# Optimization experiments

Hardware: AMD Instinct MI355X
Metric: run time of the kernel (lower is better)

The kernel has to match this reference:

```python
import jax, jax.numpy as jnp
import numpy as np

B, N, D, H, R, K = 64, 197, 768, 3072, 16, 1


def setup_inputs() -> dict:
    key = jax.random.key(0)
    ks = jax.random.split(key, 9)
    s1 = 1.0 / np.sqrt(D)
    s2 = 1.0 / np.sqrt(H)
    return {
        "x": jax.random.normal(ks[0], (B, N, D), dtype=jnp.float32),
        "W1": jax.random.normal(ks[1], (H, D), dtype=jnp.float32) * s1,
        "b1": jax.random.normal(ks[2], (H,), dtype=jnp.float32) * s1,
        "A1": jax.random.normal(ks[3], (K, R, D), dtype=jnp.float32) * s1,
        "B1": jax.random.normal(ks[4], (K, H, R), dtype=jnp.float32) * 0.01,
        "W2": jax.random.normal(ks[5], (D, H), dtype=jnp.float32) * s2,
        "b2": jax.random.normal(ks[6], (D,), dtype=jnp.float32) * s2,
        "A2": jax.random.normal(ks[7], (K, R, H), dtype=jnp.float32) * s2,
        "B2": jax.random.normal(ks[8], (K, D, R), dtype=jnp.float32) * 0.01,
    }


def _lora(x, A, Bm):
    # result of torch: (B @ (A @ x^T.unsqueeze(1))).sum(1).transpose(1,2)
    # A: [K, r, d_in], Bm: [K, d_out, r], x: [b, n, d_in] -> [b, n, d_out]
    t = jnp.einsum('krd,bnd->bknr', A, x)          # low-rank projection
    return jnp.einsum('kor,bknr->bno', Bm, t)      # expand + sum over K


def reference(x, W1, b1, A1, B1, W2, b2, A2, B2):
    # fc1 (Linear + LoRA correction)
    h = jnp.einsum('bnd,hd->bnh', x, W1) + b1 + _lora(x, A1, B1)
    # exact (erf-based) GELU, matching torch nn.GELU default
    h = jax.nn.gelu(h, approximate=False)
    # dropout p=0 and norm=Identity by default -> no-ops
    out = jnp.einsum('bnh,dh->bnd', h, W2) + b2 + _lora(h, A2, B2)
    return out
```

## Files before the change

### kernel.cpp

```cpp
#include <hip/hip_runtime.h>
#include <math.h>

#define M_ROWS 12608
#define D_DIM  768
#define H_DIM  3072

typedef __bf16 bf16_t;
typedef __bf16 bf16x8 __attribute__((ext_vector_type(8)));
typedef float  f32x4  __attribute__((ext_vector_type(4)));

__device__ __forceinline__ float gelu_fast(float v) {
  float v2 = v * v;
  float z = v * fmaf(0.044715f, v2, 1.0f);
  float e = __expf(-1.5957691216057308f * z);
  return v * __builtin_amdgcn_rcpf(1.0f + e);
}

__global__ void cast_f32_bf16_kernel(const float* __restrict__ in,
                                     bf16_t* __restrict__ out, long n) {
  long i = ((long)blockIdx.x * 256 + threadIdx.x) * 16;
  if (i + 15 < n) {
    float4 v[4];
#pragma unroll
    for (int q = 0; q < 4; ++q) v[q] = *(const float4*)(in + i + q * 4);
    bf16_t ov[16];
#pragma unroll
    for (int q = 0; q < 4; ++q) {
      ov[q * 4 + 0] = (bf16_t)v[q].x; ov[q * 4 + 1] = (bf16_t)v[q].y;
      ov[q * 4 + 2] = (bf16_t)v[q].z; ov[q * 4 + 3] = (bf16_t)v[q].w;
    }
    *(bf16x8*)(out + i) = *(bf16x8*)ov;
    *(bf16x8*)(out + i + 8) = *(bf16x8*)(ov + 8);
  } else {
    for (; i < n; ++i) out[i] = (bf16_t)in[i];
  }
}

__global__ void fold_lora_kernel(const float* __restrict__ W,
                                 const float* __restrict__ A,
                                 const float* __restrict__ Bm,
                                 bf16_t* __restrict__ Weff,
                                 int OUT, int IN) {
  const int nseg = IN >> 3;
  long idx = (long)blockIdx.x * 256 + threadIdx.x;
  if (idx >= (long)OUT * nseg) return;
  int o = (int)(idx / nseg);
  int s = (int)(idx - (long)o * nseg);
  const float* wp = W + (size_t)o * IN + s * 8;
  float4 w0 = *(const float4*)wp, w1 = *(const float4*)(wp + 4);
  float acc[8] = {w0.x, w0.y, w0.z, w0.w, w1.x, w1.y, w1.z, w1.w};
  float4 b4[4];
#pragma unroll
  for (int q = 0; q < 4; ++q) b4[q] = *(const float4*)(Bm + o * 16 + q * 4);
  const float* bb = (const float*)b4;
#pragma unroll
  for (int r = 0; r < 16; ++r) {
    float b = bb[r];
    const float* ap = A + (size_t)r * IN + s * 8;
    float4 a0 = *(const float4*)ap, a1 = *(const float4*)(ap + 4);
    acc[0] = fmaf(b, a0.x, acc[0]); acc[1] = fmaf(b, a0.y, acc[1]);
    acc[2] = fmaf(b, a0.z, acc[2]); acc[3] = fmaf(b, a0.w, acc[3]);
    acc[4] = fmaf(b, a1.x, acc[4]); acc[5] = fmaf(b, a1.y, acc[5]);
    acc[6] = fmaf(b, a1.z, acc[6]); acc[7] = fmaf(b, a1.w, acc[7]);
  }
  bf16_t ov[8];
#pragma unroll
  for (int i = 0; i < 8; ++i) ov[i] = (bf16_t)acc[i];
  *(bf16x8*)(Weff + (size_t)o * IN + s * 8) = *(bf16x8*)ov;
}

template <bool GELU, typename OutT, int SCHED>
__global__ __launch_bounds__(256, 2) void gemm_kernel(
    const bf16_t* __restrict__ Amat, const bf16_t* __restrict__ Bmat,
    const float* __restrict__ bias, OutT* __restrict__ Cmat,
    int Mrows, int Ncols, int Kd) {
  __shared__ char smem[65536];
  bf16_t* lds = (bf16_t*)smem;
  float* sT = (float*)smem;

  int rowb, colb;
  const int xcd = blockIdx.x & 7, t = blockIdx.x >> 3;
  if (SCHED == 1) {
    colb = t / 13;
    rowb = (t % 13) * 8 + xcd;
    if (rowb >= 99) return;
  } else {
    rowb = (t / 3) * 4 + (xcd & 3);
    if (rowb >= 99) return;
    colb = (xcd >> 2) * 3 + (t % 3);
  }
  const int row0 = rowb * 128, col0 = colb * 128;

  const int tid = threadIdx.x, lane = tid & 63, wave = tid >> 6;
  const int wm = wave & 1, wn = wave >> 1;

  const bf16_t* gA[4]; const bf16_t* gB[4];
  int offA[4], offB[4];
#pragma unroll
  for (int q = 0; q < 4; ++q) {
    int c = tid + q * 256;
    int r = c >> 3, kkg = c & 7;
    int ra = row0 + r; if (ra > Mrows - 1) ra = Mrows - 1;
    gA[q] = Amat + (size_t)ra * Kd + kkg * 8;
    offA[q] = r * 64 + (kkg ^ (r & 7)) * 8;
    gB[q] = Bmat + (size_t)(col0 + r) * Kd + kkg * 8;
    offB[q] = 8192 + r * 64 + (kkg ^ (r & 7)) * 8;
  }

  const int rl = lane & 15, kc = lane >> 4;
  int aoffs[4], boffs[4];
#pragma unroll
  for (int i = 0; i < 4; ++i) {
    int ra = wm * 64 + i * 16 + rl;
    int rb = wn * 64 + i * 16 + rl;
    aoffs[i] = ra * 64 + ((kc ^ (ra & 7)) * 8);
    boffs[i] = 8192 + rb * 64 + ((kc ^ (rb & 7)) * 8);
  }

  f32x4 acc[4][4] = {};
  f32x4 pA[4], pB[4];
  const int iters = Kd / 64;

#pragma unroll
  for (int q = 0; q < 4; ++q) {
    pA[q] = *(const f32x4*)gA[q]; pB[q] = *(const f32x4*)gB[q];
    gA[q] += 64; gB[q] += 64;
  }
#pragma unroll
  for (int q = 0; q < 4; ++q) {
    *(f32x4*)(lds + offA[q]) = pA[q];
    *(f32x4*)(lds + offB[q]) = pB[q];
  }

  for (int it = 0; it < iters; ++it) {
    const bool more = (it + 1 < iters);
    if (more) {
#pragma unroll
      for (int q = 0; q < 4; ++q) {
        pA[q] = *(const f32x4*)gA[q]; pB[q] = *(const f32x4*)gB[q];
        gA[q] += 64; gB[q] += 64;
      }
    }
    __syncthreads();
    const bf16_t* buf = lds + (it & 1) * 16384;
#pragma unroll
    for (int ks = 0; ks < 2; ++ks) {
      bf16x8 af[4], bfr[4];
#pragma unroll
      for (int i = 0; i < 4; ++i) af[i] = *(const bf16x8*)(buf + (aoffs[i] ^ (ks * 32)));
#pragma unroll
      for (int i = 0; i < 4; ++i) bfr[i] = *(const bf16x8*)(buf + (boffs[i] ^ (ks * 32)));
#pragma unroll
      for (int mi = 0; mi < 4; ++mi)
#pragma unroll
        for (int ni = 0; ni < 4; ++ni)
          acc[mi][ni] = __builtin_amdgcn_mfma_f32_16x16x32_bf16(
              af[mi], bfr[ni], acc[mi][ni], 0, 0, 0);
    }
    if (more) {
      bf16_t* nbuf = lds + ((it + 1) & 1) * 16384;
#pragma unroll
      for (int q = 0; q < 4; ++q) {
        *(f32x4*)(nbuf + offA[q]) = pA[q];
        *(f32x4*)(nbuf + offB[q]) = pB[q];
      }
    }
  }

  const int crow = (lane >> 4) * 4, ccol = lane & 15;
  if constexpr (GELU) {
    __syncthreads();
#pragma unroll
    for (int p = 0; p < 2; ++p) {
#pragma unroll
      for (int s = 0; s < 2; ++s) {
        int mi = 2 * p + s;
#pragma unroll
        for (int ni = 0; ni < 4; ++ni)
#pragma unroll
          for (int r = 0; r < 4; ++r)
            sT[(wm * 32 + s * 16 + crow + r) * 132 + wn * 64 + ni * 16 + ccol] =
                acc[mi][ni][r];
      }
      __syncthreads();
      const int erow = tid >> 2, eseg = tid & 3;
      const int grow = row0 + (erow >> 5) * 64 + (2 * p + ((erow >> 4) & 1)) * 16 + (erow & 15);
      if (grow < Mrows) {
        const float* src = sT + erow * 132 + eseg * 32;
        const float* bsrc = bias + col0 + eseg * 32;
        bf16_t ov[32];
#pragma unroll
        for (int i = 0; i < 32; ++i)
          ov[i] = (bf16_t)gelu_fast(src[i] + bsrc[i]);
        bf16_t* dst = (bf16_t*)Cmat + (size_t)grow * Ncols + col0 + eseg * 32;
#pragma unroll
        for (int k = 0; k < 4; ++k)
          *(bf16x8*)(dst + k * 8) = *(bf16x8*)(ov + k * 8);
      }
      __syncthreads();
    }
  } else {
#pragma unroll
    for (int ni = 0; ni < 4; ++ni) {
      const int gc = col0 + wn * 64 + ni * 16 + ccol;
      const float bv = bias[gc];
#pragma unroll
      for (int mi = 0; mi < 4; ++mi) {
        const int gr = row0 + wm * 64 + mi * 16 + crow;
#pragma unroll
        for (int r = 0; r < 4; ++r) {
          const int row = gr + r;
          if (row < Mrows)
            Cmat[(size_t)row * Ncols + gc] = acc[mi][ni][r] + bv;
        }
      }
    }
  }
}

extern "C" void kernel_launch(void* const* d_in, const int* in_sizes, int n_in,
                              void* d_out, int out_size, void* d_ws, size_t ws_size,
                              hipStream_t stream) {
  const float* x  = (const float*)d_in[0];
  const float* W1 = (const float*)d_in[1];
  const float* b1 = (const float*)d_in[2];
  const float* A1 = (const float*)d_in[3];
  const float* B1 = (const float*)d_in[4];
  const float* W2 = (const float*)d_in[5];
  const float* b2 = (const float*)d_in[6];
  const float* A2 = (const float*)d_in[7];
  const float* B2 = (const float*)d_in[8];
  float* out = (float*)d_out;

  char* ws = (char*)d_ws;
  bf16_t* xb    = (bf16_t*)ws;
  bf16_t* W1eff = (bf16_t*)(ws + 19366144);
  bf16_t* W2eff = (bf16_t*)(ws + 19366144 + 4718592);
  bf16_t* hbuf  = (bf16_t*)(ws + 19366144 + 2 * 4718592);

  const long nx = (long)M_ROWS * D_DIM;
  cast_f32_bf16_kernel<<<(int)(nx / 16 / 256 + 1), 256, 0, stream>>>(x, xb, nx);

  fold_lora_kernel<<<1152, 256, 0, stream>>>(W1, A1, B1, W1eff, H_DIM, D_DIM);
  fold_lora_kernel<<<1152, 256, 0, stream>>>(W2, A2, B2, W2eff, D_DIM, H_DIM);

  gemm_kernel<true, bf16_t, 1><<<2496, 256, 0, stream>>>(
      xb, W1eff, b1, hbuf, M_ROWS, H_DIM, D_DIM);
  gemm_kernel<false, float, 2><<<600, 256, 0, stream>>>(
      hbuf, W2eff, b2, out, M_ROWS, D_DIM, H_DIM);
}
```

Before: 319.9 us.

## Load A fragments directly from global, single-buffer B in LDS, fuse prep kernels

The GEMM now loads A-operand MFMA fragments straight from global memory into registers instead of staging them through LDS. Only B goes through LDS, now single-buffered with two barriers per iteration. That shrinks shared memory enough to raise launch bounds to 3 blocks per CU. The cast and two LoRA-fold kernels are merged into one prep launch to cut launch overhead. The risk is that uncoalesced per-lane global A loads and the extra barriers may stall the MFMA pipeline.

```diff
diff --git a/kernel.cpp b/kernel.cpp
--- a/kernel.cpp
+++ b/kernel.cpp
@@ -16,34 +16,29 @@
   return v * __builtin_amdgcn_rcpf(1.0f + e);
 }
 
-__global__ void cast_f32_bf16_kernel(const float* __restrict__ in,
-                                     bf16_t* __restrict__ out, long n) {
-  long i = ((long)blockIdx.x * 256 + threadIdx.x) * 16;
-  if (i + 15 < n) {
-    float4 v[4];
-#pragma unroll
-    for (int q = 0; q < 4; ++q) v[q] = *(const float4*)(in + i + q * 4);
-    bf16_t ov[16];
-#pragma unroll
-    for (int q = 0; q < 4; ++q) {
-      ov[q * 4 + 0] = (bf16_t)v[q].x; ov[q * 4 + 1] = (bf16_t)v[q].y;
-      ov[q * 4 + 2] = (bf16_t)v[q].z; ov[q * 4 + 3] = (bf16_t)v[q].w;
-    }
-    *(bf16x8*)(out + i) = *(bf16x8*)ov;
-    *(bf16x8*)(out + i + 8) = *(bf16x8*)(ov + 8);
-  } else {
-    for (; i < n; ++i) out[i] = (bf16_t)in[i];
-  }
-}
-
-__global__ void fold_lora_kernel(const float* __restrict__ W,
-                                 const float* __restrict__ A,
-                                 const float* __restrict__ Bm,
-                                 bf16_t* __restrict__ Weff,
-                                 int OUT, int IN) {
+__device__ __forceinline__ void cast16(const float* __restrict__ in,
+                                       bf16_t* __restrict__ out, int blk) {
+  long i = ((long)blk * 256 + threadIdx.x) * 16;
+  float4 v[4];
+#pragma unroll
+  for (int q = 0; q < 4; ++q) v[q] = *(const float4*)(in + i + q * 4);
+  bf16_t ov[16];
+#pragma unroll
+  for (int q = 0; q < 4; ++q) {
+    ov[q * 4 + 0] = (bf16_t)v[q].x; ov[q * 4 + 1] = (bf16_t)v[q].y;
+    ov[q * 4 + 2] = (bf16_t)v[q].z; ov[q * 4 + 3] = (bf16_t)v[q].w;
+  }
+  *(bf16x8*)(out + i) = *(bf16x8*)ov;
+  *(bf16x8*)(out + i + 8) = *(bf16x8*)(ov + 8);
+}
+
+__device__ __forceinline__ void fold8(const float* __restrict__ W,
+                                      const float* __restrict__ A,
+                                      const float* __restrict__ Bm,
+                                      bf16_t* __restrict__ Weff,
+                                      int IN, int blk) {
   const int nseg = IN >> 3;
-  long idx = (long)blockIdx.x * 256 + threadIdx.x;
-  if (idx >= (long)OUT * nseg) return;
+  long idx = (long)blk * 256 + threadIdx.x;
   int o = (int)(idx / nseg);
   int s = (int)(idx - (long)o * nseg);
   const float* wp = W + (size_t)o * IN + s * 8;
@@ -69,12 +64,23 @@
   *(bf16x8*)(Weff + (size_t)o * IN + s * 8) = *(bf16x8*)ov;
 }
 
-template <bool GELU, typename OutT, int SCHED>
-__global__ __launch_bounds__(256, 2) void gemm_kernel(
+__global__ void prep_kernel(const float* __restrict__ x, bf16_t* __restrict__ xb,
+                            const float* __restrict__ W1, const float* __restrict__ A1,
+                            const float* __restrict__ B1, bf16_t* __restrict__ W1eff,
+                            const float* __restrict__ W2, const float* __restrict__ A2,
+                            const float* __restrict__ B2, bf16_t* __restrict__ W2eff) {
+  int b = blockIdx.x;
+  if (b < 2364) cast16(x, xb, b);
+  else if (b < 3516) fold8(W1, A1, B1, W1eff, D_DIM, b - 2364);
+  else fold8(W2, A2, B2, W2eff, H_DIM, b - 3516);
+}
+
+template <bool GELU, typename OutT, int SCHED, int SMEM_BYTES>
+__global__ __launch_bounds__(256, 3) void gemm_kernel(
     const bf16_t* __restrict__ Amat, const bf16_t* __restrict__ Bmat,
     const float* __restrict__ bias, OutT* __restrict__ Cmat,
     int Mrows, int Ncols, int Kd) {
-  __shared__ char smem[65536];
+  __shared__ char smem[SMEM_BYTES];
   bf16_t* lds = (bf16_t*)smem;
   float* sT = (float*)smem;
 
@@ -93,77 +99,75 @@
 
   const int tid = threadIdx.x, lane = tid & 63, wave = tid >> 6;
   const int wm = wave & 1, wn = wave >> 1;
-
-  const bf16_t* gA[4]; const bf16_t* gB[4];
-  int offA[4], offB[4];
+  const int rl = lane & 15, kc = lane >> 4;
+
+  const bf16_t* aP[4];
+#pragma unroll
+  for (int mi = 0; mi < 4; ++mi) {
+    int r = row0 + wm * 64 + mi * 16 + rl;
+    if (r > Mrows - 1) r = Mrows - 1;
+    aP[mi] = Amat + (size_t)r * Kd + kc * 8;
+  }
+
+  const bf16_t* gB[4];
+  int offB[4];
 #pragma unroll
   for (int q = 0; q < 4; ++q) {
     int c = tid + q * 256;
     int r = c >> 3, kkg = c & 7;
-    int ra = row0 + r; if (ra > Mrows - 1) ra = Mrows - 1;
-    gA[q] = Amat + (size_t)ra * Kd + kkg * 8;
-    offA[q] = r * 64 + (kkg ^ (r & 7)) * 8;
     gB[q] = Bmat + (size_t)(col0 + r) * Kd + kkg * 8;
-    offB[q] = 8192 + r * 64 + (kkg ^ (r & 7)) * 8;
-  }
-
-  const int rl = lane & 15, kc = lane >> 4;
-  int aoffs[4], boffs[4];
+    offB[q] = r * 64 + (kkg ^ (r & 7)) * 8;
+  }
+
+  int boffs[4];
 #pragma unroll
   for (int i = 0; i < 4; ++i) {
-    int ra = wm * 64 + i * 16 + rl;
     int rb = wn * 64 + i * 16 + rl;
-    aoffs[i] = ra * 64 + ((kc ^ (ra & 7)) * 8);
-    boffs[i] = 8192 + rb * 64 + ((kc ^ (rb & 7)) * 8);
+    boffs[i] = rb * 64 + ((kc ^ (rb & 7)) * 8);
   }
 
   f32x4 acc[4][4] = {};
-  f32x4 pA[4], pB[4];
+  f32x4 pB[4];
   const int iters = Kd / 64;
 
 #pragma unroll
-  for (int q = 0; q < 4; ++q) {
-    pA[q] = *(const f32x4*)gA[q]; pB[q] = *(const f32x4*)gB[q];
-    gA[q] += 64; gB[q] += 64;
-  }
-#pragma unroll
-  for (int q = 0; q < 4; ++q) {
-    *(f32x4*)(lds + offA[q]) = pA[q];
-    *(f32x4*)(lds + offB[q]) = pB[q];
-  }
+  for (int q = 0; q < 4; ++q) { pB[q] = *(const f32x4*)gB[q]; gB[q] += 64; }
+#pragma unroll
+  for (int q = 0; q < 4; ++q) *(f32x4*)(lds + offB[q]) = pB[q];
+  __syncthreads();
 
   for (int it = 0; it < iters; ++it) {
     const bool more = (it + 1 < iters);
     if (more) {
 #pragma unroll
-      for (int q = 0; q < 4; ++q) {
-        pA[q] = *(const f32x4*)gA[q]; pB[q] = *(const f32x4*)gB[q];
-        gA[q] += 64; gB[q] += 64;
-      }
-    }
-    __syncthreads();
-    const bf16_t* buf = lds + (it & 1) * 16384;
+      for (int q = 0; q < 4; ++q) { pB[q] = *(const f32x4*)gB[q]; gB[q] += 64; }
+    }
+    bf16x8 af[4][2];
+#pragma unroll
+    for (int mi = 0; mi < 4; ++mi) {
+      af[mi][0] = *(const bf16x8*)(aP[mi]);
+      af[mi][1] = *(const bf16x8*)(aP[mi] + 32);
+      aP[mi] += 64;
+    }
 #pragma unroll
     for (int ks = 0; ks < 2; ++ks) {
-      bf16x8 af[4], bfr[4];
-#pragma unroll
-      for (int i = 0; i < 4; ++i) af[i] = *(const bf16x8*)(buf + (aoffs[i] ^ (ks * 32)));
-#pragma unroll
-      for (int i = 0; i < 4; ++i) bfr[i] = *(const bf16x8*)(buf + (boffs[i] ^ (ks * 32)));
+      bf16x8 bfr[4];
+#pragma unroll
+      for (int i = 0; i < 4; ++i)
+        bfr[i] = *(const bf16x8*)(lds + (boffs[i] ^ (ks * 32)));
 #pragma unroll
       for (int mi = 0; mi < 4; ++mi)
 #pragma unroll
         for (int ni = 0; ni < 4; ++ni)
           acc[mi][ni] = __builtin_amdgcn_mfma_f32_16x16x32_bf16(
-              af[mi], bfr[ni], acc[mi][ni], 0, 0, 0);
+              af[mi][ks], bfr[ni], acc[mi][ni], 0, 0, 0);
     }
     if (more) {
-      bf16_t* nbuf = lds + ((it + 1) & 1) * 16384;
-#pragma unroll
-      for (int q = 0; q < 4; ++q) {
-        *(f32x4*)(nbuf + offA[q]) = pA[q];
-        *(f32x4*)(nbuf + offB[q]) = pB[q];
-      }
+      __syncthreads();
+#pragma unroll
+      for (int q = 0; q < 4; ++q)
+        *(f32x4*)(lds + offB[q]) = pB[q];
+      __syncthreads();
     }
   }
 
@@ -238,14 +242,11 @@
   bf16_t* W2eff = (bf16_t*)(ws + 19366144 + 4718592);
   bf16_t* hbuf  = (bf16_t*)(ws + 19366144 + 2 * 4718592);
 
-  const long nx = (long)M_ROWS * D_DIM;
-  cast_f32_bf16_kernel<<<(int)(nx / 16 / 256 + 1), 256, 0, stream>>>(x, xb, nx);
-
-  fold_lora_kernel<<<1152, 256, 0, stream>>>(W1, A1, B1, W1eff, H_DIM, D_DIM);
-  fold_lora_kernel<<<1152, 256, 0, stream>>>(W2, A2, B2, W2eff, D_DIM, H_DIM);
-
-  gemm_kernel<true, bf16_t, 1><<<2496, 256, 0, stream>>>(
+  prep_kernel<<<4668, 256, 0, stream>>>(x, xb, W1, A1, B1, W1eff,
+                                        W2, A2, B2, W2eff);
+
+  gemm_kernel<true, bf16_t, 1, 33792><<<2496, 256, 0, stream>>>(
       xb, W1eff, b1, hbuf, M_ROWS, H_DIM, D_DIM);
-  gemm_kernel<false, float, 2><<<600, 256, 0, stream>>>(
+  gemm_kernel<false, float, 2, 16384><<<600, 256, 0, stream>>>(
       hbuf, W2eff, b2, out, M_ROWS, D_DIM, H_DIM);
 }
```

Result: slower. 459.4 us (+43.6%).

## Single-buffer GEMM LDS to raise occupancy and fuse prep kernels

Applied to the files above, without the earlier changes.

Merges the x cast and both LoRA fold kernels into one prep launch. The GEMM drops LDS double buffering, which cuts shared memory from 64KB to about 32KB per block, and raises the launch bounds to 3 blocks per CU. This trades the overlap of LDS writes with MFMA work for an extra barrier per K step, in return for higher occupancy and fewer launches.

```diff
diff --git a/kernel.cpp b/kernel.cpp
--- a/kernel.cpp
+++ b/kernel.cpp
@@ -16,34 +16,29 @@
   return v * __builtin_amdgcn_rcpf(1.0f + e);
 }
 
-__global__ void cast_f32_bf16_kernel(const float* __restrict__ in,
-                                     bf16_t* __restrict__ out, long n) {
-  long i = ((long)blockIdx.x * 256 + threadIdx.x) * 16;
-  if (i + 15 < n) {
-    float4 v[4];
-#pragma unroll
-    for (int q = 0; q < 4; ++q) v[q] = *(const float4*)(in + i + q * 4);
-    bf16_t ov[16];
-#pragma unroll
-    for (int q = 0; q < 4; ++q) {
-      ov[q * 4 + 0] = (bf16_t)v[q].x; ov[q * 4 + 1] = (bf16_t)v[q].y;
-      ov[q * 4 + 2] = (bf16_t)v[q].z; ov[q * 4 + 3] = (bf16_t)v[q].w;
-    }
-    *(bf16x8*)(out + i) = *(bf16x8*)ov;
-    *(bf16x8*)(out + i + 8) = *(bf16x8*)(ov + 8);
-  } else {
-    for (; i < n; ++i) out[i] = (bf16_t)in[i];
-  }
-}
-
-__global__ void fold_lora_kernel(const float* __restrict__ W,
-                                 const float* __restrict__ A,
-                                 const float* __restrict__ Bm,
-                                 bf16_t* __restrict__ Weff,
-                                 int OUT, int IN) {
+__device__ __forceinline__ void cast16(const float* __restrict__ in,
+                                       bf16_t* __restrict__ out, int blk) {
+  long i = ((long)blk * 256 + threadIdx.x) * 16;
+  float4 v[4];
+#pragma unroll
+  for (int q = 0; q < 4; ++q) v[q] = *(const float4*)(in + i + q * 4);
+  bf16_t ov[16];
+#pragma unroll
+  for (int q = 0; q < 4; ++q) {
+    ov[q * 4 + 0] = (bf16_t)v[q].x; ov[q * 4 + 1] = (bf16_t)v[q].y;
+    ov[q * 4 + 2] = (bf16_t)v[q].z; ov[q * 4 + 3] = (bf16_t)v[q].w;
+  }
+  *(bf16x8*)(out + i) = *(bf16x8*)ov;
+  *(bf16x8*)(out + i + 8) = *(bf16x8*)(ov + 8);
+}
+
+__device__ __forceinline__ void fold8(const float* __restrict__ W,
+                                      const float* __restrict__ A,
+                                      const float* __restrict__ Bm,
+                                      bf16_t* __restrict__ Weff,
+                                      int IN, int blk) {
   const int nseg = IN >> 3;
-  long idx = (long)blockIdx.x * 256 + threadIdx.x;
-  if (idx >= (long)OUT * nseg) return;
+  long idx = (long)blk * 256 + threadIdx.x;
   int o = (int)(idx / nseg);
   int s = (int)(idx - (long)o * nseg);
   const float* wp = W + (size_t)o * IN + s * 8;
@@ -69,12 +64,23 @@
   *(bf16x8*)(Weff + (size_t)o * IN + s * 8) = *(bf16x8*)ov;
 }
 
-template <bool GELU, typename OutT, int SCHED>
-__global__ __launch_bounds__(256, 2) void gemm_kernel(
+__global__ void prep_kernel(const float* __restrict__ x, bf16_t* __restrict__ xb,
+                            const float* __restrict__ W1, const float* __restrict__ A1,
+                            const float* __restrict__ B1, bf16_t* __restrict__ W1eff,
+                            const float* __restrict__ W2, const float* __restrict__ A2,
+                            const float* __restrict__ B2, bf16_t* __restrict__ W2eff) {
+  int b = blockIdx.x;
+  if (b < 2364) cast16(x, xb, b);
+  else if (b < 3516) fold8(W1, A1, B1, W1eff, D_DIM, b - 2364);
+  else fold8(W2, A2, B2, W2eff, H_DIM, b - 3516);
+}
+
+template <bool GELU, typename OutT, int SCHED, int SMEM_BYTES>
+__global__ __launch_bounds__(256, 3) void gemm_kernel(
     const bf16_t* __restrict__ Amat, const bf16_t* __restrict__ Bmat,
     const float* __restrict__ bias, OutT* __restrict__ Cmat,
     int Mrows, int Ncols, int Kd) {
-  __shared__ char smem[65536];
+  __shared__ char smem[SMEM_BYTES];
   bf16_t* lds = (bf16_t*)smem;
   float* sT = (float*)smem;
 
@@ -131,6 +137,7 @@
     *(f32x4*)(lds + offA[q]) = pA[q];
     *(f32x4*)(lds + offB[q]) = pB[q];
   }
+  __syncthreads();
 
   for (int it = 0; it < iters; ++it) {
     const bool more = (it + 1 < iters);
@@ -141,15 +148,13 @@
         gA[q] += 64; gB[q] += 64;
       }
     }
-    __syncthreads();
-    const bf16_t* buf = lds + (it & 1) * 16384;
 #pragma unroll
     for (int ks = 0; ks < 2; ++ks) {
       bf16x8 af[4], bfr[4];
 #pragma unroll
-      for (int i = 0; i < 4; ++i) af[i] = *(const bf16x8*)(buf + (aoffs[i] ^ (ks * 32)));
-#pragma unroll
-      for (int i = 0; i < 4; ++i) bfr[i] = *(const bf16x8*)(buf + (boffs[i] ^ (ks * 32)));
+      for (int i = 0; i < 4; ++i) af[i] = *(const bf16x8*)(lds + (aoffs[i] ^ (ks * 32)));
+#pragma unroll
+      for (int i = 0; i < 4; ++i) bfr[i] = *(const bf16x8*)(lds + (boffs[i] ^ (ks * 32)));
 #pragma unroll
       for (int mi = 0; mi < 4; ++mi)
 #pragma unroll
@@ -158,12 +163,13 @@
               af[mi], bfr[ni], acc[mi][ni], 0, 0, 0);
     }
     if (more) {
-      bf16_t* nbuf = lds + ((it + 1) & 1) * 16384;
+      __syncthreads();
 #pragma unroll
       for (int q = 0; q < 4; ++q) {
-        *(f32x4*)(nbuf + offA[q]) = pA[q];
-        *(f32x4*)(nbuf + offB[q]) = pB[q];
-      }
+        *(f32x4*)(lds + offA[q]) = pA[q];
+        *(f32x4*)(lds + offB[q]) = pB[q];
+      }
+      __syncthreads();
     }
   }
 
@@ -238,14 +244,11 @@
   bf16_t* W2eff = (bf16_t*)(ws + 19366144 + 4718592);
   bf16_t* hbuf  = (bf16_t*)(ws + 19366144 + 2 * 4718592);
 
-  const long nx = (long)M_ROWS * D_DIM;
-  cast_f32_bf16_kernel<<<(int)(nx / 16 / 256 + 1), 256, 0, stream>>>(x, xb, nx);
-
-  fold_lora_kernel<<<1152, 256, 0, stream>>>(W1, A1, B1, W1eff, H_DIM, D_DIM);
-  fold_lora_kernel<<<1152, 256, 0, stream>>>(W2, A2, B2, W2eff, D_DIM, H_DIM);
-
-  gemm_kernel<true, bf16_t, 1><<<2496, 256, 0, stream>>>(
+  prep_kernel<<<4668, 256, 0, stream>>>(x, xb, W1, A1, B1, W1eff,
+                                        W2, A2, B2, W2eff);
+
+  gemm_kernel<true, bf16_t, 1, 33792><<<2496, 256, 0, stream>>>(
       xb, W1eff, b1, hbuf, M_ROWS, H_DIM, D_DIM);
-  gemm_kernel<false, float, 2><<<600, 256, 0, stream>>>(
+  gemm_kernel<false, float, 2, 32768><<<600, 256, 0, stream>>>(
       hbuf, W2eff, b2, out, M_ROWS, D_DIM, H_DIM);
 }
```

Result: faster. 297.1 us (-7.1%).
